# Optimization experiments

Hardware: AMD Instinct MI355X
Metric: run time of the kernel (lower is better)

## Reference

```python
import jax, jax.numpy as jnp
import numpy as np

CHANNELS = 256
CODEBOOK_SIZE = 8192
UPDATE_SPEED = 0.01
N_TOKENS = 32768


def setup_inputs() -> dict:
    key = jax.random.key(0)
    k1, k2 = jax.random.split(key)
    embeddings = jax.random.normal(k1, (N_TOKENS, CHANNELS), dtype=jnp.float32)
    code_usage = jnp.ones((CODEBOOK_SIZE,), dtype=jnp.float32)
    code_embedding_sum = jax.random.normal(k2, (CODEBOOK_SIZE, CHANNELS), dtype=jnp.float32)
    return {"embeddings": embeddings, "code_usage": code_usage,
            "code_embedding_sum": code_embedding_sum}


def reference(embeddings, code_usage, code_embedding_sum):
    # codebook from EMA statistics: [K, C]
    codebook = code_embedding_sum / jnp.clip(code_usage, 1e-5, None)[:, None]

    # encode: nearest code by Euclidean distance. argmin over codes is
    # invariant under sqrt, so use squared distances (avoids sqrt of [K, N]).
    cb_sq = jnp.sum(codebook * codebook, axis=-1)            # [K]
    x_sq = jnp.sum(embeddings * embeddings, axis=-1)         # [N]
    # d2[k, n] = ||cb_k - x_n||^2
    d2 = cb_sq[:, None] - 2.0 * jnp.einsum('kc,nc->kn', codebook, embeddings) + x_sq[None, :]
    codes = jnp.argmin(d2, axis=0).astype(jnp.int32)         # [N]

    # decode: gather codebook rows
    quantized = jnp.take(codebook, codes, axis=0)            # [N, C]

    # straight-through estimator
    embeddings_q = embeddings + jax.lax.stop_gradient(quantized - embeddings)

    # commitment loss: mse(stop_grad(embeddings_q), embeddings)
    diff = jax.lax.stop_gradient(embeddings_q) - embeddings
    commitment_loss = jnp.mean(diff * diff)

    # EMA updates (training mode, under no_grad in the original)
    n = embeddings.shape[0]
    counts = jax.ops.segment_sum(jnp.ones((n,), dtype=code_usage.dtype),
                                 codes, num_segments=CODEBOOK_SIZE)
    emb_sum = jax.ops.segment_sum(embeddings, codes, num_segments=CODEBOOK_SIZE)
    s = jnp.float32(UPDATE_SPEED)
    new_code_usage = jax.lax.stop_gradient(code_usage * (1.0 - s) + counts * s)
    new_code_embedding_sum = jax.lax.stop_gradient(
        code_embedding_sum * (1.0 - s) + emb_sum * s)

    return codes, embeddings_q, commitment_loss, new_code_usage, new_code_embedding_sum
```

## Files before the change

kernel.cpp:

```cpp
#include <hip/hip_runtime.h>

#define CH 256
#define KC 8192
#define KCP 8448
#define NT 32768

#define TM 128
#define TN 128
#define BK 32
#define YS 3
#define JQ (KCP / YS)
#define NSTG ((JQ / TN) * (CH / BK))

typedef _Float16 half4_t __attribute__((ext_vector_type(4)));
typedef _Float16 half8_t __attribute__((ext_vector_type(8)));
typedef float floatx4 __attribute__((ext_vector_type(4)));

typedef __attribute__((address_space(1))) const unsigned int guint_t;
typedef __attribute__((address_space(3))) unsigned int luint_t;

__device__ __forceinline__ int swz(int row, int chunk) {
    return row * BK + ((chunk ^ ((row >> 1) & 3)) << 3);
}

__global__ void k_prep(const float* __restrict__ usage,
                       const float* __restrict__ ces,
                       const float* __restrict__ emb,
                       _Float16* __restrict__ cbh,
                       _Float16* __restrict__ cbl,
                       float* __restrict__ cbsq,
                       _Float16* __restrict__ eh,
                       _Float16* __restrict__ el,
                       int* __restrict__ hist,
                       unsigned long long* __restrict__ packed) {
    int b = blockIdx.x, t = threadIdx.x;
    if (b < KCP) {
        if (b < KC) {
            float uc = fmaxf(usage[b], 1e-5f);
            float v  = ces[b * CH + t];
            float cb = v / uc;
            _Float16 h = (_Float16)cb;
            cbh[b * CH + t] = h;
            cbl[b * CH + t] = (_Float16)(cb - (float)h);

            float p = cb * cb;
            #pragma unroll
            for (int off = 32; off; off >>= 1) p += __shfl_down(p, off);
            __shared__ float ps[4];
            int lane = t & 63, w = t >> 6;
            if (lane == 0) ps[w] = p;
            __syncthreads();
            if (t == 0) cbsq[b] = ps[0] + ps[1] + ps[2] + ps[3];
            if (t == 1) hist[b] = 0;
            int gid = b * CH + t;
            if (gid < NT) packed[gid] = 0xFFFFFFFFFFFFFFFFull;
        } else {
            cbh[b * CH + t] = (_Float16)0.0f;
            cbl[b * CH + t] = (_Float16)0.0f;
            if (t == 0) cbsq[b] = 3.0e38f;
        }
    } else {
        int i = (b - KCP) * 256 + t;
        float4 v = ((const float4*)emb)[i];
        float va[4] = {v.x, v.y, v.z, v.w};
        half4_t h, l;
        #pragma unroll
        for (int q = 0; q < 4; ++q) {
            _Float16 hh = (_Float16)va[q];
            h[q] = hh;
            l[q] = (_Float16)(va[q] - (float)hh);
        }
        ((half4_t*)eh)[i] = h;
        ((half4_t*)el)[i] = l;
    }
}

__launch_bounds__(256, 3)
__global__ void k_argmin(const _Float16* __restrict__ eh,
                         const _Float16* __restrict__ el,
                         const _Float16* __restrict__ cbh,
                         const _Float16* __restrict__ cbl,
                         const float* __restrict__ cbsq,
                         unsigned long long* __restrict__ packed) {
    __shared__ __align__(16) _Float16 sm[4][TM * BK];
    __shared__ float cand_v[2][TM];
    __shared__ int   cand_i[2][TM];

    const int t    = threadIdx.x;
    const int lane = t & 63;
    const int wave = t >> 6;
    const int wx   = wave & 1;
    const int wy   = wave >> 1;
    const int lr   = lane & 15;
    const int koq  = lane >> 4;

    const int n0 = blockIdx.x * TM;
    const int jq = blockIdx.y * JQ;

    const _Float16* dsrc = (wave == 0) ? eh : (wave == 1) ? el
                         : (wave == 2) ? cbh : cbl;
    const int qsw   = (lane & 3) ^ ((lane >> 3) & 3);
    const int lrow  = lane >> 2;

    float minv[16];
    int   mini[16];
    #pragma unroll
    for (int e = 0; e < 16; ++e) { minv[e] = 3.402823466e38f; mini[e] = 0; }

    floatx4 acc[4][4];
    #pragma unroll
    for (int mf = 0; mf < 4; ++mf)
        #pragma unroll
        for (int nf = 0; nf < 4; ++nf)
            acc[mf][nf] = (floatx4){0.f, 0.f, 0.f, 0.f};

    #pragma unroll 1
    for (int s = 0; s < NSTG; ++s) {
        const int c0 = (s & 7) * BK;
        const int jb = jq + (s >> 3) * TN;
        const int rb = (wave < 2) ? n0 : jb;

        {
            const _Float16* gbase = dsrc + (size_t)(rb + lrow) * CH + c0 + qsw * 8;
            #pragma unroll
            for (int i = 0; i < 8; ++i) {
                const _Float16* g = gbase + (size_t)(i * 16) * CH;
                __builtin_amdgcn_global_load_lds(
                    (guint_t*)g, (luint_t*)&sm[wave][i * 512], 16, 0, 0);
            }
        }
        __syncthreads();

        half8_t fah[4], fal[4];
        #pragma unroll
        for (int mf = 0; mf < 4; ++mf) {
            int off = swz(wy * 64 + mf * 16 + lr, koq);
            fah[mf] = *(const half8_t*)&sm[0][off];
            fal[mf] = *(const half8_t*)&sm[1][off];
        }
        #pragma unroll
        for (int nf = 0; nf < 4; ++nf) {
            int offb = swz(wx * 64 + nf * 16 + lr, koq);
            half8_t fbh = *(const half8_t*)&sm[2][offb];
            half8_t fbl = *(const half8_t*)&sm[3][offb];
            #pragma unroll
            for (int mf = 0; mf < 4; ++mf) {
                acc[mf][nf] = __builtin_amdgcn_mfma_f32_16x16x32_f16(
                    fah[mf], fbh, acc[mf][nf], 0, 0, 0);
                acc[mf][nf] = __builtin_amdgcn_mfma_f32_16x16x32_f16(
                    fah[mf], fbl, acc[mf][nf], 0, 0, 0);
                acc[mf][nf] = __builtin_amdgcn_mfma_f32_16x16x32_f16(
                    fal[mf], fbh, acc[mf][nf], 0, 0, 0);
            }
        }

        if ((s & 7) == 7) {
            int jbase = jq + (s >> 3) * TN;
            #pragma unroll
            for (int nf = 0; nf < 4; ++nf) {
                int j = jbase + wx * 64 + nf * 16 + lr;
                float sq = cbsq[j];
                #pragma unroll
                for (int mf = 0; mf < 4; ++mf) {
                    floatx4 a = acc[mf][nf];
                    #pragma unroll
                    for (int r = 0; r < 4; ++r) {
                        float sc = sq - 2.0f * a[r];
                        int e = mf * 4 + r;
                        if (sc < minv[e]) { minv[e] = sc; mini[e] = j; }
                    }
                    acc[mf][nf] = (floatx4){0.f, 0.f, 0.f, 0.f};
                }
            }
        }
        __syncthreads();
    }

    #pragma unroll
    for (int e = 0; e < 16; ++e) {
        float v = minv[e];
        int   x = mini[e];
        #pragma unroll
        for (int m = 1; m <= 8; m <<= 1) {
            float ov = __shfl_xor(v, m, 64);
            int   ox = __shfl_xor(x, m, 64);
            if (ov < v || (ov == v && ox < x)) { v = ov; x = ox; }
        }
        if (lr == 0) {
            int row = wy * 64 + (e >> 2) * 16 + (lane >> 4) * 4 + (e & 3);
            cand_v[wx][row] = v;
            cand_i[wx][row] = x;
        }
    }
    __syncthreads();

    if (t < TM) {
        float v0 = cand_v[0][t]; int i0 = cand_i[0][t];
        float v1 = cand_v[1][t]; int i1 = cand_i[1][t];
        if (v1 < v0 || (v1 == v0 && i1 < i0)) { v0 = v1; i0 = i1; }
        unsigned sb = __float_as_uint(v0);
        sb = (sb & 0x80000000u) ? ~sb : (sb | 0x80000000u);
        unsigned long long key = ((unsigned long long)sb << 32) | (unsigned)i0;
        atomicMin(&packed[n0 + t], key);
    }
}

__global__ void k_gather(const float* __restrict__ emb,
                         const float* __restrict__ ces,
                         const float* __restrict__ usage,
                         const unsigned long long* __restrict__ packed,
                         float* __restrict__ out_eq,
                         float* __restrict__ codes_f,
                         int* __restrict__ hist,
                         float* __restrict__ partials) {
    int t = threadIdx.x;
    int wave = t >> 6, lane = t & 63;
    int n = blockIdx.x * 4 + wave;
    int k = (int)(packed[n] & 0xFFFFFFFFull);
    float uc = fmaxf(usage[k], 1e-5f);
    int c = lane * 4;

    float4 e = *(const float4*)&emb[(size_t)n * CH + c];
    float4 v = *(const float4*)&ces[(size_t)k * CH + c];
    float ea[4] = {e.x, e.y, e.z, e.w};
    float va[4] = {v.x, v.y, v.z, v.w};
    float eqa[4];
    float p = 0.0f;
    #pragma unroll
    for (int q = 0; q < 4; ++q) {
        float cb = va[q] / uc;
        float eq = ea[q] + (cb - ea[q]);
        eqa[q] = eq;
        float d = eq - ea[q];
        p += d * d;
    }
    *(float4*)&out_eq[(size_t)n * CH + c] =
        (float4){eqa[0], eqa[1], eqa[2], eqa[3]};

    #pragma unroll
    for (int off = 32; off; off >>= 1) p += __shfl_down(p, off);
    __shared__ float ps[4];
    if (lane == 0) {
        ps[wave] = p;
        codes_f[n] = (float)k;
        atomicAdd(&hist[k], 1);
    }
    __syncthreads();
    if (t == 0) partials[blockIdx.x] = ps[0] + ps[1] + ps[2] + ps[3];
}

__global__ void k_scan(const int* __restrict__ hist,
                       int* __restrict__ offs,
                       int* __restrict__ cursor) {
    __shared__ int bs[256];
    int t = threadIdx.x;
    int base = t * 32;
    int loc[32];
    int s = 0;
    #pragma unroll
    for (int i = 0; i < 32; ++i) { loc[i] = s; s += hist[base + i]; }
    int mysum = s;
    bs[t] = s;
    __syncthreads();
    for (int off = 1; off < 256; off <<= 1) {
        int v = (t >= off) ? bs[t - off] : 0;
        __syncthreads();
        bs[t] += v;
        __syncthreads();
    }
    int excl = bs[t] - mysum;
    #pragma unroll
    for (int i = 0; i < 32; ++i) {
        int o = excl + loc[i];
        offs[base + i]   = o;
        cursor[base + i] = o;
    }
}

__global__ void k_scatter(const unsigned long long* __restrict__ packed,
                          int* __restrict__ cursor,
                          int* __restrict__ bucket) {
    int n = blockIdx.x * 256 + threadIdx.x;
    int k = (int)(packed[n] & 0xFFFFFFFFull);
    int pos = atomicAdd(&cursor[k], 1);
    bucket[pos] = n;
}

__global__ void k_ema(const float* __restrict__ emb,
                      const float* __restrict__ ces,
                      const float* __restrict__ usage,
                      const int* __restrict__ hist,
                      const int* __restrict__ offs,
                      const int* __restrict__ bucket,
                      float* __restrict__ out_ces,
                      float* __restrict__ out_usage) {
    const float s = 0.01f;
    const float oms = 1.0f - s;
    int k = blockIdx.x, t = threadIdx.x;
    int start = offs[k], cnt = hist[k];
    float sum = 0.0f;
    #pragma unroll 2
    for (int i = 0; i < cnt; ++i) {
        int n = bucket[start + i];
        sum += emb[(size_t)n * CH + t];
    }
    out_ces[(size_t)k * CH + t] = oms * ces[(size_t)k * CH + t] + s * sum;
    if (t == 0) out_usage[k] = oms * usage[k] + s * (float)cnt;
}

__global__ void k_final(const float* __restrict__ partials,
                        float* __restrict__ out_loss) {
    int t = threadIdx.x;
    float p = 0.0f;
    for (int i = t; i < NT / 4; i += 256) p += partials[i];
    #pragma unroll
    for (int off = 32; off; off >>= 1) p += __shfl_down(p, off);
    __shared__ float ps[4];
    if ((t & 63) == 0) ps[t >> 6] = p;
    __syncthreads();
    if (t == 0)
        out_loss[0] = (ps[0] + ps[1] + ps[2] + ps[3]) * (1.0f / 8388608.0f);
}

extern "C" void kernel_launch(void* const* d_in, const int* in_sizes, int n_in,
                              void* d_out, int out_size, void* d_ws, size_t ws_size,
                              hipStream_t stream) {
    const float* emb   = (const float*)d_in[0];
    const float* usage = (const float*)d_in[1];
    const float* ces   = (const float*)d_in[2];

    float* out      = (float*)d_out;
    float* o_codes  = out;
    float* o_eq     = out + NT;
    float* o_loss   = o_eq + (size_t)NT * CH;
    float* o_usage  = o_loss + 1;
    float* o_ces    = o_usage + KC;

    unsigned long long* packed = (unsigned long long*)d_ws;
    float* cbsq     = (float*)(packed + NT);
    float* partials = cbsq + KCP;
    int* hist   = (int*)(partials + NT / 4);
    int* offs   = hist + KC;
    int* cursor = offs + KC;
    int* bucket = cursor + KC;
    _Float16* eh  = (_Float16*)(bucket + NT);
    _Float16* el  = eh + (size_t)NT * CH;
    _Float16* cbh = el + (size_t)NT * CH;
    _Float16* cbl = cbh + (size_t)KCP * CH;

    k_prep<<<KCP + NT * CH / 1024, 256, 0, stream>>>(
        usage, ces, emb, cbh, cbl, cbsq, eh, el, hist, packed);
    dim3 agrid(NT / TM, YS);
    k_argmin<<<agrid, 256, 0, stream>>>(eh, el, cbh, cbl, cbsq, packed);
    k_gather<<<NT / 4, 256, 0, stream>>>(emb, ces, usage, packed, o_eq,
                                         o_codes, hist, partials);
    k_scan<<<1, 256, 0, stream>>>(hist, offs, cursor);
    k_scatter<<<NT / 256, 256, 0, stream>>>(packed, cursor, bucket);
    k_ema<<<KC, 256, 0, stream>>>(emb, ces, usage, hist, offs, bucket,
                                  o_ces, o_usage);
    k_final<<<1, 256, 0, stream>>>(partials, o_loss);
}
```

Measured before the change: 646.6 us.

## Drop codebook padding, split codes four ways, reduce argmin per tile into LDS

```diff
diff --git a/kernel.cpp b/kernel.cpp
--- a/kernel.cpp
+++ b/kernel.cpp
@@ -2,14 +2,13 @@
 
 #define CH 256
 #define KC 8192
-#define KCP 8448
 #define NT 32768
 
 #define TM 128
 #define TN 128
 #define BK 32
-#define YS 3
-#define JQ (KCP / YS)
+#define YS 4
+#define JQ (KC / YS)
 #define NSTG ((JQ / TN) * (CH / BK))
 
 typedef _Float16 half4_t __attribute__((ext_vector_type(4)));
@@ -34,33 +33,27 @@
                        int* __restrict__ hist,
                        unsigned long long* __restrict__ packed) {
     int b = blockIdx.x, t = threadIdx.x;
-    if (b < KCP) {
-        if (b < KC) {
-            float uc = fmaxf(usage[b], 1e-5f);
-            float v  = ces[b * CH + t];
-            float cb = v / uc;
-            _Float16 h = (_Float16)cb;
-            cbh[b * CH + t] = h;
-            cbl[b * CH + t] = (_Float16)(cb - (float)h);
-
-            float p = cb * cb;
-            #pragma unroll
-            for (int off = 32; off; off >>= 1) p += __shfl_down(p, off);
-            __shared__ float ps[4];
-            int lane = t & 63, w = t >> 6;
-            if (lane == 0) ps[w] = p;
-            __syncthreads();
-            if (t == 0) cbsq[b] = ps[0] + ps[1] + ps[2] + ps[3];
-            if (t == 1) hist[b] = 0;
-            int gid = b * CH + t;
-            if (gid < NT) packed[gid] = 0xFFFFFFFFFFFFFFFFull;
-        } else {
-            cbh[b * CH + t] = (_Float16)0.0f;
-            cbl[b * CH + t] = (_Float16)0.0f;
-            if (t == 0) cbsq[b] = 3.0e38f;
-        }
+    if (b < KC) {
+        float uc = fmaxf(usage[b], 1e-5f);
+        float v  = ces[b * CH + t];
+        float cb = v / uc;
+        _Float16 h = (_Float16)cb;
+        cbh[b * CH + t] = h;
+        cbl[b * CH + t] = (_Float16)(cb - (float)h);
+
+        float p = cb * cb;
+        #pragma unroll
+        for (int off = 32; off; off >>= 1) p += __shfl_down(p, off);
+        __shared__ float ps[4];
+        int lane = t & 63, w = t >> 6;
+        if (lane == 0) ps[w] = p;
+        __syncthreads();
+        if (t == 0) cbsq[b] = ps[0] + ps[1] + ps[2] + ps[3];
+        if (t == 1) hist[b] = 0;
+        int gid = b * CH + t;
+        if (gid < NT) packed[gid] = 0xFFFFFFFFFFFFFFFFull;
     } else {
-        int i = (b - KCP) * 256 + t;
+        int i = (b - KC) * 256 + t;
         float4 v = ((const float4*)emb)[i];
         float va[4] = {v.x, v.y, v.z, v.w};
         half4_t h, l;
@@ -75,7 +68,7 @@
     }
 }
 
-__launch_bounds__(256, 3)
+__launch_bounds__(256, 4)
 __global__ void k_argmin(const _Float16* __restrict__ eh,
                          const _Float16* __restrict__ el,
                          const _Float16* __restrict__ cbh,
@@ -99,13 +92,13 @@
 
     const _Float16* dsrc = (wave == 0) ? eh : (wave == 1) ? el
                          : (wave == 2) ? cbh : cbl;
-    const int qsw   = (lane & 3) ^ ((lane >> 3) & 3);
-    const int lrow  = lane >> 2;
-
-    float minv[16];
-    int   mini[16];
-    #pragma unroll
-    for (int e = 0; e < 16; ++e) { minv[e] = 3.402823466e38f; mini[e] = 0; }
+    const int qsw  = (lane & 3) ^ ((lane >> 3) & 3);
+    const int lrow = lane >> 2;
+
+    if (t < TM) {
+        cand_v[0][t] = 3.402823466e38f; cand_i[0][t] = 0;
+        cand_v[1][t] = 3.402823466e38f; cand_i[1][t] = 0;
+    }
 
     floatx4 acc[4][4];
     #pragma unroll
@@ -157,42 +150,44 @@
         if ((s & 7) == 7) {
             int jbase = jq + (s >> 3) * TN;
             #pragma unroll
-            for (int nf = 0; nf < 4; ++nf) {
-                int j = jbase + wx * 64 + nf * 16 + lr;
-                float sq = cbsq[j];
+            for (int np = 0; np < 2; ++np) {
+                int j0 = jbase + wx * 64 + (np * 2) * 16 + lr;
+                float sq0 = cbsq[j0];
+                float sq1 = cbsq[j0 + 16];
                 #pragma unroll
                 for (int mf = 0; mf < 4; ++mf) {
-                    floatx4 a = acc[mf][nf];
                     #pragma unroll
                     for (int r = 0; r < 4; ++r) {
-                        float sc = sq - 2.0f * a[r];
-                        int e = mf * 4 + r;
-                        if (sc < minv[e]) { minv[e] = sc; mini[e] = j; }
+                        float v0 = sq0 - 2.0f * acc[mf][np * 2][r];
+                        float v1 = sq1 - 2.0f * acc[mf][np * 2 + 1][r];
+                        float v = v0; int x = j0;
+                        if (v1 < v) { v = v1; x = j0 + 16; }
+                        #pragma unroll
+                        for (int m = 1; m <= 8; m <<= 1) {
+                            float ov = __shfl_xor(v, m, 64);
+                            int   ox = __shfl_xor(x, m, 64);
+                            if (ov < v || (ov == v && ox < x)) { v = ov; x = ox; }
+                        }
+                        if (lr == 0) {
+                            int row = wy * 64 + mf * 16 + koq * 4 + r;
+                            float cv = cand_v[wx][row];
+                            int   ci = cand_i[wx][row];
+                            if (v < cv || (v == cv && x < ci)) {
+                                cand_v[wx][row] = v;
+                                cand_i[wx][row] = x;
+                            }
+                        }
                     }
-                    acc[mf][nf] = (floatx4){0.f, 0.f, 0.f, 0.f};
                 }
             }
-        }
-        __syncthreads();
-    }
-
-    #pragma unroll
-    for (int e = 0; e < 16; ++e) {
-        float v = minv[e];
-        int   x = mini[e];
-        #pragma unroll
-        for (int m = 1; m <= 8; m <<= 1) {
-            float ov = __shfl_xor(v, m, 64);
-            int   ox = __shfl_xor(x, m, 64);
-            if (ov < v || (ov == v && ox < x)) { v = ov; x = ox; }
-        }
-        if (lr == 0) {
-            int row = wy * 64 + (e >> 2) * 16 + (lane >> 4) * 4 + (e & 3);
-            cand_v[wx][row] = v;
-            cand_i[wx][row] = x;
-        }
-    }
-    __syncthreads();
+            #pragma unroll
+            for (int mf = 0; mf < 4; ++mf)
+                #pragma unroll
+                for (int nf = 0; nf < 4; ++nf)
+                    acc[mf][nf] = (floatx4){0.f, 0.f, 0.f, 0.f};
+        }
+        __syncthreads();
+    }
 
     if (t < TM) {
         float v0 = cand_v[0][t]; int i0 = cand_i[0][t];
@@ -293,10 +288,24 @@
                       const int* __restrict__ offs,
                       const int* __restrict__ bucket,
                       float* __restrict__ out_ces,
-                      float* __restrict__ out_usage) {
+                      float* __restrict__ out_usage,
+                      const float* __restrict__ partials,
+                      float* __restrict__ out_loss) {
+    int k = blockIdx.x, t = threadIdx.x;
+    if (k == KC) {
+        float p = 0.0f;
+        for (int i = t; i < NT / 4; i += 256) p += partials[i];
+        #pragma unroll
+        for (int off = 32; off; off >>= 1) p += __shfl_down(p, off);
+        __shared__ float ps[4];
+        if ((t & 63) == 0) ps[t >> 6] = p;
+        __syncthreads();
+        if (t == 0)
+            out_loss[0] = (ps[0] + ps[1] + ps[2] + ps[3]) * (1.0f / 8388608.0f);
+        return;
+    }
     const float s = 0.01f;
     const float oms = 1.0f - s;
-    int k = blockIdx.x, t = threadIdx.x;
     int start = offs[k], cnt = hist[k];
     float sum = 0.0f;
     #pragma unroll 2
@@ -308,20 +317,6 @@
     if (t == 0) out_usage[k] = oms * usage[k] + s * (float)cnt;
 }
 
-__global__ void k_final(const float* __restrict__ partials,
-                        float* __restrict__ out_loss) {
-    int t = threadIdx.x;
-    float p = 0.0f;
-    for (int i = t; i < NT / 4; i += 256) p += partials[i];
-    #pragma unroll
-    for (int off = 32; off; off >>= 1) p += __shfl_down(p, off);
-    __shared__ float ps[4];
-    if ((t & 63) == 0) ps[t >> 6] = p;
-    __syncthreads();
-    if (t == 0)
-        out_loss[0] = (ps[0] + ps[1] + ps[2] + ps[3]) * (1.0f / 8388608.0f);
-}
-
 extern "C" void kernel_launch(void* const* d_in, const int* in_sizes, int n_in,
                               void* d_out, int out_size, void* d_ws, size_t ws_size,
                               hipStream_t stream) {
@@ -338,7 +333,7 @@
 
     unsigned long long* packed = (unsigned long long*)d_ws;
     float* cbsq     = (float*)(packed + NT);
-    float* partials = cbsq + KCP;
+    float* partials = cbsq + KC;
     int* hist   = (int*)(partials + NT / 4);
     int* offs   = hist + KC;
     int* cursor = offs + KC;
@@ -346,9 +341,9 @@
     _Float16* eh  = (_Float16*)(bucket + NT);
     _Float16* el  = eh + (size_t)NT * CH;
     _Float16* cbh = el + (size_t)NT * CH;
-    _Float16* cbl = cbh + (size_t)KCP * CH;
-
-    k_prep<<<KCP + NT * CH / 1024, 256, 0, stream>>>(
+    _Float16* cbl = cbh + (size_t)KC * CH;
+
+    k_prep<<<KC + NT * CH / 1024, 256, 0, stream>>>(
         usage, ces, emb, cbh, cbl, cbsq, eh, el, hist, packed);
     dim3 agrid(NT / TM, YS);
     k_argmin<<<agrid, 256, 0, stream>>>(eh, el, cbh, cbl, cbsq, packed);
@@ -356,7 +351,6 @@
                                          o_codes, hist, partials);
     k_scan<<<1, 256, 0, stream>>>(hist, offs, cursor);
     k_scatter<<<NT / 256, 256, 0, stream>>>(packed, cursor, bucket);
-    k_ema<<<KC, 256, 0, stream>>>(emb, ces, usage, hist, offs, bucket,
-                                  o_ces, o_usage);
-    k_final<<<1, 256, 0, stream>>>(partials, o_loss);
-}
+    k_ema<<<KC + 1, 256, 0, stream>>>(emb, ces, usage, hist, offs, bucket,
+                                      o_ces, o_usage, partials, o_loss);
+}
```

New measurement: 792.0 us. 22.5% more time.
